# Optimization experiments

Hardware: AMD Instinct MI355X
Metric: run time of the kernel (lower is better)

## Reference

```python
import jax, jax.numpy as jnp
import numpy as np
from jax import lax


def _cor(x):
    # Per-sample centered cross-correlation of channel 2 with its own 11x11
    # center crop (scipy.ndimage.correlate, mode='constant', cval=0, origin=0).
    # The torch code detaches x before this step, so gradients do not flow.
    x = lax.stop_gradient(x)
    ch = x[:, 2]                      # [B, 28, 28]
    tmpl = ch[:, 8:19, 8:19]          # [B, 11, 11]

    def one(im, k):
        # lax.conv is cross-correlation (no kernel flip); pad 5 => 'same' 28x28
        return lax.conv_general_dilated(im[None, None], k[None, None],
                                        (1, 1), [(5, 5), (5, 5)])[0, 0]

    return jax.vmap(one)(ch, tmpl)[:, None]  # [B, 1, 28, 28]


def _conv(x, w, b):
    return lax.conv_general_dilated(x, w, (1, 1), 'VALID') + b[None, :, None, None]


def _maxpool2(x):
    return lax.reduce_window(x, -jnp.inf, lax.max, (1, 1, 2, 2), (1, 1, 2, 2), 'VALID')


def setup_inputs() -> dict:
    key = jax.random.key(0)
    ks = jax.random.split(key, 7)
    B = 8192
    x = jax.random.normal(ks[0], (B, 3, 28, 28), dtype=jnp.float32)
    w1 = jax.random.normal(ks[1], (32, 1, 5, 5), dtype=jnp.float32) * 0.1
    b1 = jax.random.normal(ks[2], (32,), dtype=jnp.float32) * 0.1
    w2 = jax.random.normal(ks[3], (64, 32, 5, 5), dtype=jnp.float32) * 0.05
    b2 = jax.random.normal(ks[4], (64,), dtype=jnp.float32) * 0.1
    w3 = jax.random.normal(ks[5], (10, 64, 3, 3), dtype=jnp.float32) * 0.05
    b3 = jax.random.normal(ks[6], (10,), dtype=jnp.float32) * 0.1
    return {"x": x, "w1": w1, "b1": b1, "w2": w2, "b2": b2, "w3": w3, "b3": b3}


def reference(x, w1, b1, w2, b2, w3, b3):
    h = _cor(x)                      # [B, 1, 28, 28]
    h = jax.nn.relu(_conv(h, w1, b1))  # [B, 32, 24, 24]
    h = _maxpool2(h)                   # [B, 32, 12, 12]
    h = jax.nn.relu(_conv(h, w2, b2))  # [B, 64, 8, 8]
    h = _maxpool2(h)                   # [B, 64, 4, 4]
    h = jax.nn.relu(_conv(h, w3, b3))  # [B, 10, 2, 2]
    h = jnp.mean(h, axis=(2, 3))       # GAP (AvgPool2d 2x2 stride 1 on 2x2) -> [B, 10]
    return jax.nn.log_softmax(h, axis=1)
```

## Files before the change

### kernel.cpp

```cpp
#include <hip/hip_runtime.h>
#include <hip/hip_bf16.h>
#include <math.h>


#define B_STRIDE 2352

typedef _Float16 f16x8 __attribute__((ext_vector_type(8)));
typedef _Float16 f16x4 __attribute__((ext_vector_type(4)));
typedef _Float16 f16x2 __attribute__((ext_vector_type(2)));
typedef float f32x4 __attribute__((ext_vector_type(4)));

#define K1_WAVES 8
#define K1_ROUNDS 2
__global__ __launch_bounds__(512, 4) void k1_cor_conv1_pool(
    const float* __restrict__ x, const float* __restrict__ w1,
    const float* __restrict__ b1, _Float16* __restrict__ out1h)
{
    __shared__ float PAD[K1_WAVES][1444];
    __shared__ float COR[K1_WAVES][784];
    __shared__ _Float16 AW1[2 * 64 * 8];
    __shared__ float b1s[32];

    const int tid = threadIdx.x;
    const int wave = tid >> 6;
    const int lane = tid & 63;

    for (int e = tid; e < 1024; e += 512) {
        const int ln = (e >> 3) & 63;
        const int oc = ((e >> 9) << 4) + (ln & 15);
        const int k = ((ln >> 4) << 3) + (e & 7);
        AW1[e] = (k < 25) ? (_Float16)w1[oc * 25 + k] : (_Float16)0.f;
    }
    if (tid < 32) b1s[tid] = b1[tid];
    __syncthreads();

    const int g = lane >> 4;
    const int c = lane & 15;
    int off[8];
#pragma unroll
    for (int jj = 0; jj < 8; ++jj) {
        const int k = g * 8 + jj;
        const int ky = k / 5;
        off[jj] = (k < 25) ? (ky * 28 + (k - ky * 5)) : 0;
    }
    const f16x8 af0 = *(const f16x8*)&AW1[lane * 8];
    const f16x8 af1 = *(const f16x8*)&AW1[(64 + lane) * 8];
    float bia0[4], bia1[4];
#pragma unroll
    for (int rr = 0; rr < 4; ++rr) {
        bia0[rr] = b1s[g * 4 + rr];
        bia1[rr] = b1s[16 + g * 4 + rr];
    }
    const int yy = lane >> 1;
    const int x0 = (lane & 1) * 14;
    float* padw = &PAD[wave][0];
    float* corw = &COR[wave][0];

    for (int r = 0; r < K1_ROUNDS; ++r) {
        const int img = blockIdx.x * (K1_WAVES * K1_ROUNDS) + r * K1_WAVES + wave;

        for (int i = lane; i < 361; i += 64)
            ((f32x4*)padw)[i] = (f32x4){0.f, 0.f, 0.f, 0.f};
        const float* xb = x + (size_t)img * B_STRIDE + 1568;
        for (int i = lane; i < 196; i += 64) {
            const float4 v = ((const float4*)xb)[i];
            const int yv = i / 7;
            float* d = &padw[(5 + yv) * 38 + 5 + (i - yv * 7) * 4];
            d[0] = v.x; d[1] = v.y; d[2] = v.z; d[3] = v.w;
        }

        if (yy < 28) {
            float a[14];
#pragma unroll
            for (int t = 0; t < 14; ++t) a[t] = 0.f;
#pragma unroll
            for (int ky = 0; ky < 11; ++ky) {
                const float* prow = &padw[(yy + ky) * 38 + x0];
                float rr2[24];
#pragma unroll
                for (int t2 = 0; t2 < 12; ++t2) {
                    const float2 v2 = ((const float2*)prow)[t2];
                    rr2[2 * t2] = v2.x; rr2[2 * t2 + 1] = v2.y;
                }
                const float* trow = &padw[(13 + ky) * 38 + 13];
#pragma unroll
                for (int kx = 0; kx < 11; ++kx) {
                    const float w = trow[kx];
#pragma unroll
                    for (int t = 0; t < 14; ++t)
                        a[t] = fmaf(rr2[kx + t], w, a[t]);
                }
            }
            float* cw = &corw[yy * 28 + x0];
#pragma unroll
            for (int t2 = 0; t2 < 7; ++t2) {
                const float2 v2 = {a[2 * t2], a[2 * t2 + 1]};
                ((float2*)cw)[t2] = v2;
            }
        }

        _Float16* outw = out1h + (size_t)img * 4608;
#pragma unroll
        for (int jq = 0; jq < 9; ++jq) {
            const int pp = jq * 16 + c;
            const int py = pp / 12, px = pp - py * 12;
            f32x4 pm0, pm1;
#pragma unroll
            for (int q = 0; q < 4; ++q) {
                const int base = (2 * py + (q >> 1)) * 28 + 2 * px + (q & 1);
                f16x8 bf;
#pragma unroll
                for (int jj = 0; jj < 8; ++jj)
                    bf[jj] = (_Float16)corw[base + off[jj]];
                const f32x4 z = {0.f, 0.f, 0.f, 0.f};
                const f32x4 d0 = __builtin_amdgcn_mfma_f32_16x16x32_f16(af0, bf, z, 0, 0, 0);
                const f32x4 d1 = __builtin_amdgcn_mfma_f32_16x16x32_f16(af1, bf, z, 0, 0, 0);
                if (q == 0) { pm0 = d0; pm1 = d1; }
                else {
#pragma unroll
                    for (int rr = 0; rr < 4; ++rr) {
                        pm0[rr] = fmaxf(pm0[rr], d0[rr]);
                        pm1[rr] = fmaxf(pm1[rr], d1[rr]);
                    }
                }
            }
            f16x4 s0, s1;
#pragma unroll
            for (int rr = 0; rr < 4; ++rr) {
                s0[rr] = (_Float16)fmaxf(pm0[rr] + bia0[rr], 0.f);
                s1[rr] = (_Float16)fmaxf(pm1[rr] + bia1[rr], 0.f);
            }
            _Float16* dsth = outw + pp * 32 + g * 4;
            *(f16x4*)dsth = s0;
            *(f16x4*)(dsth + 16) = s1;
        }
    }
}

#define K2_ROUNDS 8
__global__ __launch_bounds__(512, 2) void k2_conv2_pool_mfma(
    const _Float16* __restrict__ in1h, const float* __restrict__ w2,
    const float* __restrict__ b2, float* __restrict__ out2)
{
    __shared__ __align__(16) _Float16 AW[25 * 4 * 64 * 8];
    __shared__ __align__(16) _Float16 XT[4][4 * 144 * 8];
    __shared__ float b2s[64];

    const int tid = threadIdx.x;
    const int wave = tid >> 6;
    const int lane = tid & 63;
    const int widx = wave >> 1;
    const int half = wave & 1;
    const int jb = half * 2;

    for (int it = 0; it < 50; ++it) {
        const int flat = it * 512 + tid;
        const int rest = (flat * 5243) >> 17;
        const int kpos = flat - rest * 25;
        const int oc = rest >> 4, icp = rest & 15;
        const float* gsrc = w2 + oc * 800 + icp * 50 + kpos;
        const f16x2 v = { (_Float16)gsrc[0], (_Float16)gsrc[25] };
        const int lane_w = (oc & 15) + (icp >> 2) * 16;
        const int idx = (((kpos * 4 + (oc >> 4)) * 64) + lane_w) * 8 + (icp & 3) * 2;
        *(f16x2*)&AW[idx] = v;
    }
    if (tid < 64) b2s[tid] = b2[tid];

    const int b0 = blockIdx.x * (4 * K2_ROUNDS);
    const int hi = (lane >> 3) & 1;
    const int ox = lane & 7;
    const int icg = lane >> 4;
    _Float16* xtw = &XT[widx][0];

    for (int r = 0; r < K2_ROUNDS; ++r) {
        __syncthreads();
        const int img = b0 + r * 4 + widx;

        const _Float16* srch = in1h + (size_t)img * 4608;
        for (int p = lane + half * 64; p < 144; p += 128) {
            const f16x8* s8 = (const f16x8*)(srch + p * 32);
#pragma unroll
            for (int ig = 0; ig < 4; ++ig)
                *(f16x8*)&xtw[(ig * 144 + p) * 8] = s8[ig];
        }
        __syncthreads();

        f32x4 acc[4][2];
#pragma unroll
        for (int i = 0; i < 4; ++i)
#pragma unroll
            for (int jj = 0; jj < 2; ++jj)
                acc[i][jj] = (f32x4){0.f, 0.f, 0.f, 0.f};

        const int prow = hi * 12 + ox;
#pragma unroll
        for (int kpos = 0; kpos < 25; ++kpos) {
            const int ky = kpos / 5, kx = kpos % 5;
            f16x8 af[4], bf[2];
#pragma unroll
            for (int i = 0; i < 4; ++i)
                af[i] = *(const f16x8*)&AW[(((kpos * 4 + i) * 64) + lane) * 8];
#pragma unroll
            for (int jj = 0; jj < 2; ++jj) {
                const int p = prow + (2 * (jb + jj) + ky) * 12 + kx;
                bf[jj] = *(const f16x8*)&xtw[(icg * 144 + p) * 8];
            }
#pragma unroll
            for (int i = 0; i < 4; ++i)
#pragma unroll
                for (int jj = 0; jj < 2; ++jj)
                    acc[i][jj] = __builtin_amdgcn_mfma_f32_16x16x32_f16(
                        af[i], bf[jj], acc[i][jj], 0, 0, 0);
        }

        float* dst = out2 + (size_t)img * 1024;
#pragma unroll
        for (int i = 0; i < 4; ++i)
#pragma unroll
            for (int jj = 0; jj < 2; ++jj)
#pragma unroll
                for (int rr = 0; rr < 4; ++rr) {
                    const int oc = i * 16 + (lane >> 4) * 4 + rr;
                    float v = fmaxf(acc[i][jj][rr] + b2s[oc], 0.f);
                    v = fmaxf(v, __shfl_xor(v, 1));
                    v = fmaxf(v, __shfl_xor(v, 8));
                    if ((lane & 9) == 0)
                        dst[oc * 16 + (jb + jj) * 4 + (ox >> 1)] = v;
                }
    }
}

__global__ __launch_bounds__(256) void k3_conv3_head(
    const float* __restrict__ in2, const float* __restrict__ w3,
    const float* __restrict__ b3, float* __restrict__ out)
{
    __shared__ float w3s[10 * 577];
    __shared__ float b3s[10];
    __shared__ float xin[4 * 1024];
    __shared__ float lg[4][16];

    const int tid = threadIdx.x;
    const int b0 = blockIdx.x * 4;

    for (int i = tid; i < 5760; i += 256)
        w3s[(i / 576) * 577 + (i % 576)] = w3[i];
    if (tid < 10) b3s[tid] = b3[tid];
    const float* src = in2 + (size_t)b0 * 1024;
    for (int i = tid; i < 1024; i += 256)
        ((float4*)xin)[i] = ((const float4*)src)[i];
    __syncthreads();

    const int img = tid >> 6;
    const int lane = tid & 63;
    const int oc = lane >> 2;
    const int pos = lane & 3;
    float v = 0.f;
    if (oc < 10) {
        const int oy = pos >> 1, oxx = pos & 1;
        const float* xi = &xin[img * 1024 + oy * 4 + oxx];
        const float* wr = &w3s[oc * 577];
        float a = 0.f;
        for (int ic = 0; ic < 64; ++ic) {
            const float* xc = xi + ic * 16;
            const float* wc = wr + ic * 9;
#pragma unroll
            for (int ky = 0; ky < 3; ++ky)
#pragma unroll
                for (int kx = 0; kx < 3; ++kx)
                    a = fmaf(xc[ky * 4 + kx], wc[ky * 3 + kx], a);
        }
        v = fmaxf(a + b3s[oc], 0.f);
    }
    v += __shfl_xor(v, 1);
    v += __shfl_xor(v, 2);
    v *= 0.25f;
    if (pos == 0 && oc < 10) lg[img][oc] = v;
    __syncthreads();
    if (lane == 0) {
        float mx = -1e30f;
        for (int i = 0; i < 10; ++i) mx = fmaxf(mx, lg[img][i]);
        float s = 0.f;
        for (int i = 0; i < 10; ++i) s += expf(lg[img][i] - mx);
        const float lse = mx + logf(s);
        float* o = out + (size_t)(b0 + img) * 10;
        for (int i = 0; i < 10; ++i) o[i] = lg[img][i] - lse;
    }
}

extern "C" void kernel_launch(void* const* d_in, const int* in_sizes, int n_in,
                              void* d_out, int out_size, void* d_ws, size_t ws_size,
                              hipStream_t stream)
{
    const float* x  = (const float*)d_in[0];
    const float* w1 = (const float*)d_in[1];
    const float* b1 = (const float*)d_in[2];
    const float* w2 = (const float*)d_in[3];
    const float* b2 = (const float*)d_in[4];
    const float* w3 = (const float*)d_in[5];
    const float* b3 = (const float*)d_in[6];
    float* out = (float*)d_out;

    const int B = in_sizes[0] / B_STRIDE;
    _Float16* pool1h = (_Float16*)d_ws;
    float* pool2 = (float*)((char*)d_ws + (size_t)B * 4608 * 2);

    k1_cor_conv1_pool<<<B / (K1_WAVES * K1_ROUNDS), 512, 0, stream>>>(x, w1, b1, pool1h);
    k2_conv2_pool_mfma<<<B / (4 * K2_ROUNDS), 512, 0, stream>>>(pool1h, w2, b2, pool2);
    k3_conv3_head<<<B / 4, 256, 0, stream>>>(pool2, w3, b3, out);
}
```

Before: 298.7 us.

## Store correlation in fp16, pipeline conv2 with per-wave ring buffer, restructure conv3 head

The correlation map in kernel 1 is now kept in shared memory as fp16, which halves LDS traffic and removes the per-element conversion before building MFMA operands. Kernel 2 now gives each wave a whole image, stages it through a circular 8-row shared buffer in two halves, and prefetches the next image into registers while the current one is computing, in place of the old block-wide syncs. Kernel 3 handles several images per block, one wave per image, splits input channels across lanes with shuffle reductions, and does the softmax across all lanes. This restructuring adds register pressure and relies on subtle ring-buffer indexing with no barriers between a wave's own LDS writes and reads.

```diff
diff --git a/kernel.cpp b/kernel.cpp
--- a/kernel.cpp
+++ b/kernel.cpp
@@ -17,7 +17,7 @@
     const float* __restrict__ b1, _Float16* __restrict__ out1h)
 {
     __shared__ float PAD[K1_WAVES][1444];
-    __shared__ float COR[K1_WAVES][784];
+    __shared__ _Float16 COR[K1_WAVES][784];
     __shared__ _Float16 AW1[2 * 64 * 8];
     __shared__ float b1s[32];
 
@@ -54,7 +54,7 @@
     const int yy = lane >> 1;
     const int x0 = (lane & 1) * 14;
     float* padw = &PAD[wave][0];
-    float* corw = &COR[wave][0];
+    _Float16* corw = &COR[wave][0];
 
     for (int r = 0; r < K1_ROUNDS; ++r) {
         const int img = blockIdx.x * (K1_WAVES * K1_ROUNDS) + r * K1_WAVES + wave;
@@ -91,11 +91,11 @@
                         a[t] = fmaf(rr2[kx + t], w, a[t]);
                 }
             }
-            float* cw = &corw[yy * 28 + x0];
+            _Float16* cw = &corw[yy * 28 + x0];
 #pragma unroll
             for (int t2 = 0; t2 < 7; ++t2) {
-                const float2 v2 = {a[2 * t2], a[2 * t2 + 1]};
-                ((float2*)cw)[t2] = v2;
+                f16x2 v2 = {(_Float16)a[2 * t2], (_Float16)a[2 * t2 + 1]};
+                *(f16x2*)&cw[2 * t2] = v2;
             }
         }
 
@@ -111,7 +111,7 @@
                 f16x8 bf;
 #pragma unroll
                 for (int jj = 0; jj < 8; ++jj)
-                    bf[jj] = (_Float16)corw[base + off[jj]];
+                    bf[jj] = corw[base + off[jj]];
                 const f32x4 z = {0.f, 0.f, 0.f, 0.f};
                 const f32x4 d0 = __builtin_amdgcn_mfma_f32_16x16x32_f16(af0, bf, z, 0, 0, 0);
                 const f32x4 d1 = __builtin_amdgcn_mfma_f32_16x16x32_f16(af1, bf, z, 0, 0, 0);
@@ -137,21 +137,18 @@
     }
 }
 
-#define K2_ROUNDS 8
+#define K2_ROUNDS 4
 __global__ __launch_bounds__(512, 2) void k2_conv2_pool_mfma(
     const _Float16* __restrict__ in1h, const float* __restrict__ w2,
     const float* __restrict__ b2, float* __restrict__ out2)
 {
     __shared__ __align__(16) _Float16 AW[25 * 4 * 64 * 8];
-    __shared__ __align__(16) _Float16 XT[4][4 * 144 * 8];
+    __shared__ __align__(16) _Float16 XT[8][4 * 96 * 8];
     __shared__ float b2s[64];
 
     const int tid = threadIdx.x;
     const int wave = tid >> 6;
     const int lane = tid & 63;
-    const int widx = wave >> 1;
-    const int half = wave & 1;
-    const int jb = half * 2;
 
     for (int it = 0; it < 50; ++it) {
         const int flat = it * 512 + tid;
@@ -166,124 +163,197 @@
     }
     if (tid < 64) b2s[tid] = b2[tid];
 
-    const int b0 = blockIdx.x * (4 * K2_ROUNDS);
+    const int b0 = blockIdx.x * (8 * K2_ROUNDS);
     const int hi = (lane >> 3) & 1;
     const int ox = lane & 7;
     const int icg = lane >> 4;
-    _Float16* xtw = &XT[widx][0];
+    _Float16* xtw = &XT[wave][0];
+
+    f16x8 ld1[6], ld2[3];
+    {
+        const _Float16* src = in1h + (size_t)(b0 + wave) * 4608;
+#pragma unroll
+        for (int cc = 0; cc < 6; ++cc)
+            ld1[cc] = *(const f16x8*)(src + lane * 48 + cc * 8);
+#pragma unroll
+        for (int cc = 0; cc < 3; ++cc)
+            ld2[cc] = *(const f16x8*)(src + 3072 + lane * 24 + cc * 8);
+    }
+    __syncthreads();
 
     for (int r = 0; r < K2_ROUNDS; ++r) {
-        __syncthreads();
-        const int img = b0 + r * 4 + widx;
-
-        const _Float16* srch = in1h + (size_t)img * 4608;
-        for (int p = lane + half * 64; p < 144; p += 128) {
-            const f16x8* s8 = (const f16x8*)(srch + p * 32);
-#pragma unroll
-            for (int ig = 0; ig < 4; ++ig)
-                *(f16x8*)&xtw[(ig * 144 + p) * 8] = s8[ig];
-        }
-        __syncthreads();
-
-        f32x4 acc[4][2];
+        const int img = b0 + r * 8 + wave;
+
+#pragma unroll
+        for (int cc = 0; cc < 6; ++cc) {
+            const int gb = lane * 96 + cc * 16;
+            const int pos = gb >> 6;
+            const int r12 = (pos * 2731) >> 15;
+            const int col = pos - r12 * 12;
+            *(f16x8*)&xtw[((((gb >> 4) & 3) * 96) + (r12 & 7) * 12 + col) * 8] = ld1[cc];
+        }
+
+        f32x4 acc[4][4];
 #pragma unroll
         for (int i = 0; i < 4; ++i)
 #pragma unroll
-            for (int jj = 0; jj < 2; ++jj)
-                acc[i][jj] = (f32x4){0.f, 0.f, 0.f, 0.f};
-
-        const int prow = hi * 12 + ox;
+            for (int j = 0; j < 4; ++j)
+                acc[i][j] = (f32x4){0.f, 0.f, 0.f, 0.f};
+
 #pragma unroll
         for (int kpos = 0; kpos < 25; ++kpos) {
-            const int ky = kpos / 5, kx = kpos % 5;
-            f16x8 af[4], bf[2];
+            const int ky = kpos / 5, kx = kpos - (kpos / 5) * 5;
+            f16x8 af[4];
 #pragma unroll
             for (int i = 0; i < 4; ++i)
                 af[i] = *(const f16x8*)&AW[(((kpos * 4 + i) * 64) + lane) * 8];
-#pragma unroll
-            for (int jj = 0; jj < 2; ++jj) {
-                const int p = prow + (2 * (jb + jj) + ky) * 12 + kx;
-                bf[jj] = *(const f16x8*)&xtw[(icg * 144 + p) * 8];
-            }
+            const f16x8 bf0 = *(const f16x8*)&xtw[(icg * 96 + ((hi + 0 + ky) & 7) * 12 + ox + kx) * 8];
+            const f16x8 bf1 = *(const f16x8*)&xtw[(icg * 96 + ((hi + 2 + ky) & 7) * 12 + ox + kx) * 8];
+#pragma unroll
+            for (int i = 0; i < 4; ++i) {
+                acc[i][0] = __builtin_amdgcn_mfma_f32_16x16x32_f16(af[i], bf0, acc[i][0], 0, 0, 0);
+                acc[i][1] = __builtin_amdgcn_mfma_f32_16x16x32_f16(af[i], bf1, acc[i][1], 0, 0, 0);
+            }
+        }
+
+#pragma unroll
+        for (int cc = 0; cc < 3; ++cc) {
+            const int gb = 6144 + lane * 48 + cc * 16;
+            const int pos = gb >> 6;
+            const int r12 = (pos * 2731) >> 15;
+            const int col = pos - r12 * 12;
+            *(f16x8*)&xtw[((((gb >> 4) & 3) * 96) + (r12 & 7) * 12 + col) * 8] = ld2[cc];
+        }
+
+        {
+            const int img_pf = b0 + ((r + 1) & (K2_ROUNDS - 1)) * 8 + wave;
+            const _Float16* src = in1h + (size_t)img_pf * 4608;
+#pragma unroll
+            for (int cc = 0; cc < 6; ++cc)
+                ld1[cc] = *(const f16x8*)(src + lane * 48 + cc * 8);
+#pragma unroll
+            for (int cc = 0; cc < 3; ++cc)
+                ld2[cc] = *(const f16x8*)(src + 3072 + lane * 24 + cc * 8);
+        }
+
+#pragma unroll
+        for (int kpos = 0; kpos < 25; ++kpos) {
+            const int ky = kpos / 5, kx = kpos - (kpos / 5) * 5;
+            f16x8 af[4];
 #pragma unroll
             for (int i = 0; i < 4; ++i)
-#pragma unroll
-                for (int jj = 0; jj < 2; ++jj)
-                    acc[i][jj] = __builtin_amdgcn_mfma_f32_16x16x32_f16(
-                        af[i], bf[jj], acc[i][jj], 0, 0, 0);
+                af[i] = *(const f16x8*)&AW[(((kpos * 4 + i) * 64) + lane) * 8];
+            const f16x8 bf2 = *(const f16x8*)&xtw[(icg * 96 + ((hi + 4 + ky) & 7) * 12 + ox + kx) * 8];
+            const f16x8 bf3 = *(const f16x8*)&xtw[(icg * 96 + ((hi + 6 + ky) & 7) * 12 + ox + kx) * 8];
+#pragma unroll
+            for (int i = 0; i < 4; ++i) {
+                acc[i][2] = __builtin_amdgcn_mfma_f32_16x16x32_f16(af[i], bf2, acc[i][2], 0, 0, 0);
+                acc[i][3] = __builtin_amdgcn_mfma_f32_16x16x32_f16(af[i], bf3, acc[i][3], 0, 0, 0);
+            }
         }
 
         float* dst = out2 + (size_t)img * 1024;
 #pragma unroll
         for (int i = 0; i < 4; ++i)
 #pragma unroll
-            for (int jj = 0; jj < 2; ++jj)
+            for (int j = 0; j < 4; ++j)
 #pragma unroll
                 for (int rr = 0; rr < 4; ++rr) {
                     const int oc = i * 16 + (lane >> 4) * 4 + rr;
-                    float v = fmaxf(acc[i][jj][rr] + b2s[oc], 0.f);
+                    float v = fmaxf(acc[i][j][rr] + b2s[oc], 0.f);
                     v = fmaxf(v, __shfl_xor(v, 1));
                     v = fmaxf(v, __shfl_xor(v, 8));
                     if ((lane & 9) == 0)
-                        dst[oc * 16 + (jb + jj) * 4 + (ox >> 1)] = v;
+                        dst[oc * 16 + j * 4 + (ox >> 1)] = v;
                 }
     }
 }
 
-__global__ __launch_bounds__(256) void k3_conv3_head(
+#define K3_ROUNDS 4
+__global__ __launch_bounds__(512, 4) void k3_conv3_head(
     const float* __restrict__ in2, const float* __restrict__ w3,
     const float* __restrict__ b3, float* __restrict__ out)
 {
-    __shared__ float w3s[10 * 577];
-    __shared__ float b3s[10];
-    __shared__ float xin[4 * 1024];
-    __shared__ float lg[4][16];
+    __shared__ float w3s[5760];
+    __shared__ float b3s[16];
+    __shared__ float xin[8][64 * 17];
 
     const int tid = threadIdx.x;
-    const int b0 = blockIdx.x * 4;
-
-    for (int i = tid; i < 5760; i += 256)
-        w3s[(i / 576) * 577 + (i % 576)] = w3[i];
+    const int wave = tid >> 6;
+    const int lane = tid & 63;
+
+    for (int i = tid; i < 5760; i += 512) w3s[i] = w3[i];
     if (tid < 10) b3s[tid] = b3[tid];
-    const float* src = in2 + (size_t)b0 * 1024;
-    for (int i = tid; i < 1024; i += 256)
-        ((float4*)xin)[i] = ((const float4*)src)[i];
     __syncthreads();
 
-    const int img = tid >> 6;
-    const int lane = tid & 63;
-    const int oc = lane >> 2;
+    const int icq = lane >> 2;
     const int pos = lane & 3;
-    float v = 0.f;
-    if (oc < 10) {
-        const int oy = pos >> 1, oxx = pos & 1;
-        const float* xi = &xin[img * 1024 + oy * 4 + oxx];
-        const float* wr = &w3s[oc * 577];
-        float a = 0.f;
-        for (int ic = 0; ic < 64; ++ic) {
-            const float* xc = xi + ic * 16;
-            const float* wc = wr + ic * 9;
+    const int oy = pos >> 1, oxx = pos & 1;
+    float* xw = &xin[wave][0];
+
+    for (int r = 0; r < K3_ROUNDS; ++r) {
+        const int img = blockIdx.x * (8 * K3_ROUNDS) + r * 8 + wave;
+
+        {
+            const float4* s4 = (const float4*)(in2 + (size_t)img * 1024 + lane * 16);
+            const float4 v0 = s4[0], v1 = s4[1], v2 = s4[2], v3 = s4[3];
+            float* d = &xw[lane * 17];
+            d[0] = v0.x;  d[1] = v0.y;  d[2] = v0.z;  d[3] = v0.w;
+            d[4] = v1.x;  d[5] = v1.y;  d[6] = v1.z;  d[7] = v1.w;
+            d[8] = v2.x;  d[9] = v2.y;  d[10] = v2.z; d[11] = v2.w;
+            d[12] = v3.x; d[13] = v3.y; d[14] = v3.z; d[15] = v3.w;
+        }
+
+        float xv[4][9];
+#pragma unroll
+        for (int il = 0; il < 4; ++il) {
+            const float* xc = &xw[(icq * 4 + il) * 17 + oy * 4 + oxx];
 #pragma unroll
             for (int ky = 0; ky < 3; ++ky)
 #pragma unroll
                 for (int kx = 0; kx < 3; ++kx)
-                    a = fmaf(xc[ky * 4 + kx], wc[ky * 3 + kx], a);
-        }
-        v = fmaxf(a + b3s[oc], 0.f);
-    }
-    v += __shfl_xor(v, 1);
-    v += __shfl_xor(v, 2);
-    v *= 0.25f;
-    if (pos == 0 && oc < 10) lg[img][oc] = v;
-    __syncthreads();
-    if (lane == 0) {
-        float mx = -1e30f;
-        for (int i = 0; i < 10; ++i) mx = fmaxf(mx, lg[img][i]);
+                    xv[il][ky * 3 + kx] = xc[ky * 4 + kx];
+        }
+        float acc[10];
+#pragma unroll
+        for (int oc = 0; oc < 10; ++oc) {
+            float a = 0.f;
+#pragma unroll
+            for (int il = 0; il < 4; ++il) {
+                const float* wc = &w3s[oc * 576 + (icq * 4 + il) * 9];
+#pragma unroll
+                for (int t = 0; t < 9; ++t)
+                    a = fmaf(xv[il][t], wc[t], a);
+            }
+            acc[oc] = a;
+        }
+
+        float lv[10];
+#pragma unroll
+        for (int oc = 0; oc < 10; ++oc) {
+            float v = acc[oc];
+            v += __shfl_xor(v, 4);
+            v += __shfl_xor(v, 8);
+            v += __shfl_xor(v, 16);
+            v += __shfl_xor(v, 32);
+            v = fmaxf(v + b3s[oc], 0.f);
+            v += __shfl_xor(v, 1);
+            v += __shfl_xor(v, 2);
+            lv[oc] = v * 0.25f;
+        }
+
+        float mx = lv[0];
+#pragma unroll
+        for (int oc = 1; oc < 10; ++oc) mx = fmaxf(mx, lv[oc]);
         float s = 0.f;
-        for (int i = 0; i < 10; ++i) s += expf(lg[img][i] - mx);
+#pragma unroll
+        for (int oc = 0; oc < 10; ++oc) s += expf(lv[oc] - mx);
         const float lse = mx + logf(s);
-        float* o = out + (size_t)(b0 + img) * 10;
-        for (int i = 0; i < 10; ++i) o[i] = lg[img][i] - lse;
+        if (lane == 0) {
+            float* o = out + (size_t)img * 10;
+#pragma unroll
+            for (int oc = 0; oc < 10; ++oc) o[oc] = lv[oc] - lse;
+        }
     }
 }
 
@@ -305,6 +375,6 @@
     float* pool2 = (float*)((char*)d_ws + (size_t)B * 4608 * 2);
 
     k1_cor_conv1_pool<<<B / (K1_WAVES * K1_ROUNDS), 512, 0, stream>>>(x, w1, b1, pool1h);
-    k2_conv2_pool_mfma<<<B / (4 * K2_ROUNDS), 512, 0, stream>>>(pool1h, w2, b2, pool2);
-    k3_conv3_head<<<B / 4, 256, 0, stream>>>(pool2, w3, b3, out);
+    k2_conv2_pool_mfma<<<B / (8 * K2_ROUNDS), 512, 0, stream>>>(pool1h, w2, b2, pool2);
+    k3_conv3_head<<<B / (8 * K3_ROUNDS), 512, 0, stream>>>(pool2, w3, b3, out);
 }
```

Result: slower. 773.4 us (+158.9%).
